# Kernel optimization log

Measured on AMD Instinct MI355X. Metric: run time of the kernel, lower is better.

## Reference

```python
import jax, jax.numpy as jnp
import numpy as np

N_ATOMS = 20000
N_PAIRS = 640000
C = 64        # channel width (pp/pi/ii nodes)
NB = 4        # number of radial basis functions


def setup_inputs() -> dict:
    key = jax.random.key(0)
    ks = jax.random.split(key, 24)
    s = 0.05  # keep tanh pre-activations in linear-ish regime
    inp = {
        "ind_2": jax.random.randint(ks[0], (N_PAIRS, 2), 0, N_ATOMS, dtype=jnp.int64)
                 if jax.config.jax_enable_x64 else
                 jax.random.randint(ks[0], (N_PAIRS, 2), 0, N_ATOMS, dtype=jnp.int32),
        "p1": jax.random.normal(ks[1], (N_ATOMS, C), jnp.float32),
        "p3": jax.random.normal(ks[2], (N_ATOMS, 3, C), jnp.float32),
        "diff": jax.random.normal(ks[3], (N_PAIRS, 3), jnp.float32),
        "basis": jax.random.uniform(ks[4], (N_PAIRS, NB), jnp.float32),
        # pp1: FFLayer([C, C], tanh, bias)
        "Wpp1a": jax.random.normal(ks[5], (C, C), jnp.float32) * s,
        "bpp1a": jnp.zeros((C,), jnp.float32),
        "Wpp1b": jax.random.normal(ks[6], (C, C), jnp.float32) * s,
        "bpp1b": jnp.zeros((C,), jnp.float32),
        # pi1: FFLayer([C, C*NB], tanh, bias), input = concat(p1_i, p1_j) -> 2C
        "Wpi1": jax.random.normal(ks[7], (2 * C, C), jnp.float32) * s,
        "bpi1": jnp.zeros((C,), jnp.float32),
        "Wpi2": jax.random.normal(ks[8], (C, C * NB), jnp.float32) * s,
        "bpi2": jnp.zeros((C * NB,), jnp.float32),
        # ii1: FFLayer([C, 3*C], tanh, no bias)
        "Wii1": jax.random.normal(ks[9], (C, C), jnp.float32) * s,
        "Wii2": jax.random.normal(ks[10], (C, 3 * C), jnp.float32) * s,
        # pp3: FFLayer([C, C], linear, no bias)
        "Wpp3a": jax.random.normal(ks[11], (C, C), jnp.float32) * s,
        "Wpp3b": jax.random.normal(ks[12], (C, C), jnp.float32) * s,
        # PIX (weighted): two biasless Dense(C)
        "Wpxi": jax.random.normal(ks[13], (C, C), jnp.float32) * s,
        "Wpxj": jax.random.normal(ks[14], (C, C), jnp.float32) * s,
        # DotLayer (weighted): two biasless Dense(C)
        "Wdi": jax.random.normal(ks[15], (C, C), jnp.float32) * s,
        "Wdj": jax.random.normal(ks[16], (C, C), jnp.float32) * s,
    }
    return inp


def reference(ind_2, p1, p3, diff, basis,
              Wpp1a, bpp1a, Wpp1b, bpp1b,
              Wpi1, bpi1, Wpi2, bpi2,
              Wii1, Wii2, Wpp3a, Wpp3b,
              Wpxi, Wpxj, Wdi, Wdj):
    n_atoms = p1.shape[0]
    i, j = ind_2[:, 0], ind_2[:, 1]

    # pp1: FFLayer (tanh, bias)
    p1h = jnp.tanh(p1 @ Wpp1a + bpp1a)
    p1h = jnp.tanh(p1h @ Wpp1b + bpp1b)

    # PILayer: gather pair endpoints, concat, FF, contract with basis
    inter = jnp.concatenate([p1h[i], p1h[j]], axis=-1)          # (P, 2C)
    inter = jnp.tanh(inter @ Wpi1 + bpi1)                        # (P, C)
    inter = jnp.tanh(inter @ Wpi2 + bpi2)                        # (P, C*NB)
    nb = basis.shape[-1]
    i1 = jnp.einsum('pcb,pb->pc', inter.reshape(-1, Wpi2.shape[-1] // nb, nb), basis)

    # ii1: FFLayer (tanh, no bias), last width 3*C
    i1 = jnp.tanh(i1 @ Wii1)
    i1 = jnp.tanh(i1 @ Wii2)                                     # (P, 3C)
    i1_1, i1_2, i1_3 = jnp.split(i1, 3, axis=-1)

    # ip1: scatter-sum interactions onto center atoms
    p1_new = jax.ops.segment_sum(i1_2, i, num_segments=n_atoms)  # (N, C)

    # pp3: linear biasless FF on equivariant channel dim
    p3h = (p3 @ Wpp3a) @ Wpp3b                                   # (N, 3, C)

    # PIX (weighted): wi(p3_i) + wj(p3_j)
    i3 = p3h[i] @ Wpxi + p3h[j] @ Wpxj                           # (P, 3, C)

    # scale by i1_3, add displacement channel scaled by i1_1
    i3 = i3 * i1_3[:, None, :] + diff[:, :, None] * i1_1[:, None, :]

    # ip3: scatter-sum equivariant interactions
    p3_new = jax.ops.segment_sum(i3, i, num_segments=n_atoms)    # (N, 3, C)

    # weighted dot product over the Cartesian axis
    dot = jnp.einsum('ixr,ixr->ir', p3_new @ Wdi, p3_new @ Wdj)  # (N, C)
    p1t1 = dot + p1_new
    p3t1 = p3_new * p1t1[:, None, :]
    return p1t1, p3t1
```

## Files before the change

### kernel.cpp

```cpp
#include <hip/hip_runtime.h>


typedef _Float16 half8 __attribute__((ext_vector_type(8)));
typedef __fp16 half2t __attribute__((ext_vector_type(2)));
typedef float floatx4 __attribute__((ext_vector_type(4)));

#define MFMA16(a, b, c) __builtin_amdgcn_mfma_f32_16x16x32_f16((a), (b), (c), 0, 0, 0)

#define WSA_OFF 0
#define W3_OFF 98304
#define P1H_OFF 114688
#define P3H_OFF 2674688
#define CNT_OFF 10354688
#define FILL_OFF 10435584
#define OFF_OFF 10516480
#define BSUM_OFF 10597376
#define IIS_OFF 13157888
#define JJS_OFF 15717888
#define BAS_OFF 18277888
#define DIF_OFF 28517888

#define FB_PI1 0
#define FB_PI2 16
#define FB_II1 48
#define FB_II2 56
#define FB_PXI 80
#define FB_PXJ 88

__device__ __forceinline__ float fast_tanh(float x) {
    float t = __expf(2.0f * x);
    return 1.0f - __fdividef(2.0f, t + 1.0f);
}

__device__ __forceinline__ floatx4 tanh4(floatx4 v) {
    floatx4 r;
    r[0] = fast_tanh(v[0]); r[1] = fast_tanh(v[1]);
    r[2] = fast_tanh(v[2]); r[3] = fast_tanh(v[3]);
    return r;
}

__device__ __forceinline__ void pack_can(const floatx4 h[4], half8& lo, half8& hi) {
    half2t dw[8];
#pragma unroll
    for (int t = 0; t < 4; ++t) {
        dw[2 * t]     = __builtin_amdgcn_cvt_pkrtz(h[t][0], h[t][1]);
        dw[2 * t + 1] = __builtin_amdgcn_cvt_pkrtz(h[t][2], h[t][3]);
    }
    union U { half8 v; half2t d[4]; } u;
    u.d[0] = dw[0]; u.d[1] = dw[1]; u.d[2] = dw[2]; u.d[3] = dw[3]; lo = u.v;
    u.d[0] = dw[4]; u.d[1] = dw[5]; u.d[2] = dw[6]; u.d[3] = dw[7]; hi = u.v;
}

__global__ __launch_bounds__(64) void k_pack(
    const float* __restrict__ Wpi1, const float* __restrict__ Wpi2,
    const float* __restrict__ Wii1, const float* __restrict__ Wii2,
    const float* __restrict__ Wpxi, const float* __restrict__ Wpxj,
    _Float16* __restrict__ wsA) {
    int f = blockIdx.x, l = threadIdx.x;
    int q = l >> 4, c15 = l & 15;
    const float* W; int ldn, mt, kb, mode;
    if (f < 16)      { W = Wpi1; ldn = 64;  mt = f >> 2;        kb = f & 3;        mode = 0; }
    else if (f < 48) { W = Wpi2; ldn = 256; mt = (f - 16) >> 1; kb = (f - 16) & 1; mode = 1; }
    else if (f < 56) { W = Wii1; ldn = 64;  mt = (f - 48) >> 1; kb = (f - 48) & 1; mode = 2; }
    else if (f < 80) { W = Wii2; ldn = 192; mt = (f - 56) >> 1; kb = (f - 56) & 1; mode = 1; }
    else if (f < 88) { W = Wpxi; ldn = 64;  mt = (f - 80) >> 1; kb = (f - 80) & 1; mode = 0; }
    else             { W = Wpxj; ldn = 64;  mt = (f - 88) >> 1; kb = (f - 88) & 1; mode = 0; }
#pragma unroll
    for (int e = 0; e < 8; ++e) {
        int k;
        if (mode == 0) k = 32 * kb + 8 * q + e;
        else if (mode == 1) {
            int d = e >> 1, h = e & 1, j = 4 * kb + d;
            k = 16 * (j >> 1) + 4 * q + 2 * (j & 1) + h;
        } else k = 4 * (8 * kb + e) + q;
        wsA[f * 512 + l * 8 + e] = (_Float16)W[k * ldn + 16 * mt + c15];
    }
}

__global__ __launch_bounds__(256) void k_w3(const float* __restrict__ A,
                                            const float* __restrict__ B,
                                            float* __restrict__ W3) {
    int t = threadIdx.x;
#pragma unroll
    for (int e = 0; e < 16; ++e) {
        int idx = t * 16 + e;
        int k = idx >> 6, c = idx & 63;
        float s = 0.f;
        for (int m = 0; m < 64; ++m) s = fmaf(A[k * 64 + m], B[m * 64 + c], s);
        W3[idx] = s;
    }
}

__device__ __forceinline__ void store8(float* dst, const float v[8]) {
    *(float4*)(dst)     = make_float4(v[0], v[1], v[2], v[3]);
    *(float4*)(dst + 4) = make_float4(v[4], v[5], v[6], v[7]);
}
__device__ __forceinline__ void fma8(const float* row, float wv, float acc[8]) {
    float4 x0 = *(const float4*)(row);
    float4 x1 = *(const float4*)(row + 4);
    acc[0] = fmaf(x0.x, wv, acc[0]); acc[1] = fmaf(x0.y, wv, acc[1]);
    acc[2] = fmaf(x0.z, wv, acc[2]); acc[3] = fmaf(x0.w, wv, acc[3]);
    acc[4] = fmaf(x1.x, wv, acc[4]); acc[5] = fmaf(x1.y, wv, acc[5]);
    acc[6] = fmaf(x1.z, wv, acc[6]); acc[7] = fmaf(x1.w, wv, acc[7]);
}

__global__ __launch_bounds__(256) void k_p1h(const float* __restrict__ p1,
                                             const float* __restrict__ Wa,
                                             const float* __restrict__ ba,
                                             const float* __restrict__ Wb,
                                             const float* __restrict__ bb,
                                             _Float16* __restrict__ p1h) {
    __shared__ float act[4][64][8];
    const int w = threadIdx.x >> 6, lane = threadIdx.x & 63;
    const int a0 = blockIdx.x * 32 + w * 8;
    {
        float t[8];
#pragma unroll
        for (int p = 0; p < 8; ++p) t[p] = p1[(a0 + p) * 64 + lane];
        store8(&act[w][lane][0], t);
    }
    __syncthreads();
    float acc[8];
    {
        float bv = ba[lane];
#pragma unroll
        for (int p = 0; p < 8; ++p) acc[p] = bv;
        for (int k = 0; k < 64; ++k) fma8(&act[w][k][0], Wa[k * 64 + lane], acc);
    }
    __syncthreads();
    {
        float t[8];
#pragma unroll
        for (int p = 0; p < 8; ++p) t[p] = fast_tanh(acc[p]);
        store8(&act[w][lane][0], t);
    }
    __syncthreads();
    {
        float bv = bb[lane];
#pragma unroll
        for (int p = 0; p < 8; ++p) acc[p] = bv;
        for (int k = 0; k < 64; ++k) fma8(&act[w][k][0], Wb[k * 64 + lane], acc);
    }
#pragma unroll
    for (int p = 0; p < 8; ++p) p1h[(a0 + p) * 64 + lane] = (_Float16)fast_tanh(acc[p]);
}

__global__ __launch_bounds__(256) void k_rowmm(const float* __restrict__ X,
                                               const float* __restrict__ W,
                                               _Float16* __restrict__ Y) {
    __shared__ float act[4][64][8];
    const int w = threadIdx.x >> 6, lane = threadIdx.x & 63;
    const int r0 = blockIdx.x * 32 + w * 8;
    {
        float t[8];
#pragma unroll
        for (int p = 0; p < 8; ++p) t[p] = X[(r0 + p) * 64 + lane];
        store8(&act[w][lane][0], t);
    }
    __syncthreads();
    float acc[8];
#pragma unroll
    for (int p = 0; p < 8; ++p) acc[p] = 0.f;
    for (int k = 0; k < 64; ++k) fma8(&act[w][k][0], W[k * 64 + lane], acc);
#pragma unroll
    for (int p = 0; p < 8; ++p) Y[(r0 + p) * 64 + lane] = (_Float16)acc[p];
}

__global__ __launch_bounds__(256) void k_hist(const int* __restrict__ ind,
                                              int* __restrict__ cnt, int n) {
    int t = blockIdx.x * 256 + threadIdx.x;
    if (t < n) atomicAdd(&cnt[ind[2 * t]], 1);
}

__global__ __launch_bounds__(256) void k_scan1(const int* __restrict__ cnt,
                                               int* __restrict__ off,
                                               int* __restrict__ bsum, int n) {
    __shared__ int s[256];
    int b = blockIdx.x, t = threadIdx.x, a = b * 256 + t;
    int v = (a < n) ? cnt[a] : 0;
    s[t] = v;
    __syncthreads();
    for (int o = 1; o < 256; o <<= 1) {
        int x = (t >= o) ? s[t - o] : 0;
        __syncthreads();
        s[t] += x;
        __syncthreads();
    }
    off[a] = s[t] - v;
    if (t == 255) bsum[b] = s[255];
}

__global__ __launch_bounds__(64) void k_scan2(int* __restrict__ bsum, int nb) {
    if (threadIdx.x == 0) {
        int r = 0;
        for (int b = 0; b < nb; ++b) { int t = bsum[b]; bsum[b] = r; r += t; }
    }
}

__global__ __launch_bounds__(256) void k_scan3(int* __restrict__ off,
                                               const int* __restrict__ bsum) {
    int a = blockIdx.x * 256 + threadIdx.x;
    off[a] += bsum[blockIdx.x];
}

__global__ __launch_bounds__(256) void k_scatter(const int* __restrict__ ind,
                                                 const int* __restrict__ off,
                                                 int* __restrict__ fill,
                                                 const float* __restrict__ basis,
                                                 const float* __restrict__ diff,
                                                 int* __restrict__ iiS,
                                                 int* __restrict__ jjS,
                                                 float4* __restrict__ basS,
                                                 float4* __restrict__ difS, int n) {
    int t = blockIdx.x * 256 + threadIdx.x;
    if (t < n) {
        int i = ind[2 * t];
        int slot = off[i] + atomicAdd(&fill[i], 1);
        iiS[slot] = i;
        jjS[slot] = ind[2 * t + 1];
        basS[slot] = *(const float4*)(basis + 4 * t);
        difS[slot] = make_float4(diff[3 * t], diff[3 * t + 1], diff[3 * t + 2], 0.f);
    }
}

__global__ __launch_bounds__(64) void k_pairs_s(
    const int* __restrict__ iiS, const int* __restrict__ jjS,
    const float4* __restrict__ basS, const float4* __restrict__ difS,
    const _Float16* __restrict__ p1h, const _Float16* __restrict__ p3h,
    const _Float16* __restrict__ wsA,
    const float* __restrict__ bpi1, const float* __restrict__ bpi2,
    float* __restrict__ outp1, float* __restrict__ outp3) {
    __shared__ float xpose[2][16][68];
    const int lane = threadIdx.x;
    const int p = lane & 15, q = lane >> 4;
    const int sb0 = blockIdx.x * 32;
    const int slot0 = sb0 + p, slot1 = sb0 + 16 + p;
    const int iA0 = iiS[slot0], jA0 = jjS[slot0];
    const int iA1 = iiS[slot1], jA1 = jjS[slot1];

    const half8* A = (const half8*)wsA;

    half8 b1[2][4];
    b1[0][0] = *(const half8*)(p1h + iA0 * 64 + q * 8);
    b1[0][1] = *(const half8*)(p1h + iA0 * 64 + 32 + q * 8);
    b1[0][2] = *(const half8*)(p1h + jA0 * 64 + q * 8);
    b1[0][3] = *(const half8*)(p1h + jA0 * 64 + 32 + q * 8);
    b1[1][0] = *(const half8*)(p1h + iA1 * 64 + q * 8);
    b1[1][1] = *(const half8*)(p1h + iA1 * 64 + 32 + q * 8);
    b1[1][2] = *(const half8*)(p1h + jA1 * 64 + q * 8);
    b1[1][3] = *(const half8*)(p1h + jA1 * 64 + 32 + q * 8);

    floatx4 h1[2][4];
#pragma unroll
    for (int mt = 0; mt < 4; ++mt) {
        floatx4 acc0 = *(const floatx4*)(bpi1 + 16 * mt + 4 * q);
        floatx4 acc1 = acc0;
#pragma unroll
        for (int kb = 0; kb < 4; ++kb) {
            half8 aw = A[(FB_PI1 + mt * 4 + kb) * 64 + lane];
            acc0 = MFMA16(aw, b1[0][kb], acc0);
            acc1 = MFMA16(aw, b1[1][kb], acc1);
        }
        h1[0][mt] = tanh4(acc0);
        h1[1][mt] = tanh4(acc1);
    }

    half8 b2lo[2], b2hi[2];
    pack_can(h1[0], b2lo[0], b2hi[0]);
    pack_can(h1[1], b2lo[1], b2hi[1]);
    float4 bsv0 = basS[slot0], bsv1 = basS[slot1];
    float i1v[2][16];
#pragma unroll
    for (int mt = 0; mt < 16; ++mt) {
        half8 a0 = A[(FB_PI2 + mt * 2 + 0) * 64 + lane];
        half8 a1 = A[(FB_PI2 + mt * 2 + 1) * 64 + lane];
        floatx4 acc0 = *(const floatx4*)(bpi2 + 16 * mt + 4 * q);
        floatx4 acc1 = acc0;
        acc0 = MFMA16(a0, b2lo[0], acc0);
        acc1 = MFMA16(a0, b2lo[1], acc1);
        acc0 = MFMA16(a1, b2hi[0], acc0);
        acc1 = MFMA16(a1, b2hi[1], acc1);
        i1v[0][mt] = fast_tanh(acc0[0]) * bsv0.x + fast_tanh(acc0[1]) * bsv0.y +
                     fast_tanh(acc0[2]) * bsv0.z + fast_tanh(acc0[3]) * bsv0.w;
        i1v[1][mt] = fast_tanh(acc1[0]) * bsv1.x + fast_tanh(acc1[1]) * bsv1.y +
                     fast_tanh(acc1[2]) * bsv1.z + fast_tanh(acc1[3]) * bsv1.w;
    }

    half8 bi[2][2];
#pragma unroll
    for (int g = 0; g < 2; ++g) {
        half2t dw[8];
#pragma unroll
        for (int j = 0; j < 8; ++j)
            dw[j] = __builtin_amdgcn_cvt_pkrtz(i1v[g][2 * j], i1v[g][2 * j + 1]);
        union U { half8 v; half2t d[4]; } u;
        u.d[0] = dw[0]; u.d[1] = dw[1]; u.d[2] = dw[2]; u.d[3] = dw[3]; bi[g][0] = u.v;
        u.d[0] = dw[4]; u.d[1] = dw[5]; u.d[2] = dw[6]; u.d[3] = dw[7]; bi[g][1] = u.v;
    }
    floatx4 h3[2][4];
#pragma unroll
    for (int mt = 0; mt < 4; ++mt) {
        half8 a0 = A[(FB_II1 + mt * 2 + 0) * 64 + lane];
        half8 a1 = A[(FB_II1 + mt * 2 + 1) * 64 + lane];
        floatx4 acc0 = {0.f, 0.f, 0.f, 0.f};
        floatx4 acc1 = {0.f, 0.f, 0.f, 0.f};
        acc0 = MFMA16(a0, bi[0][0], acc0);
        acc1 = MFMA16(a0, bi[1][0], acc1);
        acc0 = MFMA16(a1, bi[0][1], acc0);
        acc1 = MFMA16(a1, bi[1][1], acc1);
        h3[0][mt] = tanh4(acc0);
        h3[1][mt] = tanh4(acc1);
    }

    half8 b4lo[2], b4hi[2];
    pack_can(h3[0], b4lo[0], b4hi[0]);
    pack_can(h3[1], b4lo[1], b4hi[1]);
    floatx4 i11v[2][4], i13v[2][4];
#pragma unroll
    for (int mt = 0; mt < 12; ++mt) {
        half8 a0 = A[(FB_II2 + mt * 2 + 0) * 64 + lane];
        half8 a1 = A[(FB_II2 + mt * 2 + 1) * 64 + lane];
        floatx4 acc0 = {0.f, 0.f, 0.f, 0.f};
        floatx4 acc1 = {0.f, 0.f, 0.f, 0.f};
        acc0 = MFMA16(a0, b4lo[0], acc0);
        acc1 = MFMA16(a0, b4lo[1], acc1);
        acc0 = MFMA16(a1, b4hi[0], acc0);
        acc1 = MFMA16(a1, b4hi[1], acc1);
        floatx4 t0 = tanh4(acc0);
        floatx4 t1 = tanh4(acc1);
        if (mt < 4) { i11v[0][mt] = t0; i11v[1][mt] = t1; }
        else if (mt < 8) {
            int g4 = ((mt - 4) * 4 + q) * 4;
            *(float4*)&xpose[0][p][g4] = make_float4(t0[0], t0[1], t0[2], t0[3]);
            *(float4*)&xpose[1][p][g4] = make_float4(t1[0], t1[1], t1[2], t1[3]);
        } else { i13v[0][mt - 8] = t0; i13v[1][mt - 8] = t1; }
    }

#pragma unroll
    for (int g = 0; g < 2; ++g) {
        float racc = xpose[g][0][lane];
        int cur = iiS[sb0 + g * 16];
#pragma unroll
        for (int pp = 1; pp < 16; ++pp) {
            int aw = iiS[sb0 + g * 16 + pp];
            if (aw != cur) {
                atomicAdd(&outp1[cur * 64 + lane], racc);
                racc = 0.f; cur = aw;
            }
            racc += xpose[g][pp][lane];
        }
        atomicAdd(&outp1[cur * 64 + lane], racc);
    }

    float4 dv0 = difS[slot0], dv1 = difS[slot1];
    float dvs[2][3] = {{dv0.x, dv0.y, dv0.z}, {dv1.x, dv1.y, dv1.z}};
#pragma unroll
    for (int x = 0; x < 3; ++x) {
        half8 bfi[2][2], bfj[2][2];
#pragma unroll
        for (int kb = 0; kb < 2; ++kb) {
            bfi[0][kb] = *(const half8*)(p3h + (iA0 * 3 + x) * 64 + kb * 32 + q * 8);
            bfj[0][kb] = *(const half8*)(p3h + (jA0 * 3 + x) * 64 + kb * 32 + q * 8);
            bfi[1][kb] = *(const half8*)(p3h + (iA1 * 3 + x) * 64 + kb * 32 + q * 8);
            bfj[1][kb] = *(const half8*)(p3h + (jA1 * 3 + x) * 64 + kb * 32 + q * 8);
        }
#pragma unroll
        for (int mt = 0; mt < 4; ++mt) {
            half8 ai0 = A[(FB_PXI + mt * 2 + 0) * 64 + lane];
            half8 ai1 = A[(FB_PXI + mt * 2 + 1) * 64 + lane];
            half8 aj0 = A[(FB_PXJ + mt * 2 + 0) * 64 + lane];
            half8 aj1 = A[(FB_PXJ + mt * 2 + 1) * 64 + lane];
            floatx4 acc0 = {0.f, 0.f, 0.f, 0.f};
            floatx4 acc1 = {0.f, 0.f, 0.f, 0.f};
            acc0 = MFMA16(ai0, bfi[0][0], acc0);
            acc1 = MFMA16(ai0, bfi[1][0], acc1);
            acc0 = MFMA16(ai1, bfi[0][1], acc0);
            acc1 = MFMA16(ai1, bfi[1][1], acc1);
            acc0 = MFMA16(aj0, bfj[0][0], acc0);
            acc1 = MFMA16(aj0, bfj[1][0], acc1);
            acc0 = MFMA16(aj1, bfj[0][1], acc0);
            acc1 = MFMA16(aj1, bfj[1][1], acc1);
            float4 v0, v1;
            v0.x = fmaf(acc0[0], i13v[0][mt][0], dvs[0][x] * i11v[0][mt][0]);
            v0.y = fmaf(acc0[1], i13v[0][mt][1], dvs[0][x] * i11v[0][mt][1]);
            v0.z = fmaf(acc0[2], i13v[0][mt][2], dvs[0][x] * i11v[0][mt][2]);
            v0.w = fmaf(acc0[3], i13v[0][mt][3], dvs[0][x] * i11v[0][mt][3]);
            v1.x = fmaf(acc1[0], i13v[1][mt][0], dvs[1][x] * i11v[1][mt][0]);
            v1.y = fmaf(acc1[1], i13v[1][mt][1], dvs[1][x] * i11v[1][mt][1]);
            v1.z = fmaf(acc1[2], i13v[1][mt][2], dvs[1][x] * i11v[1][mt][2]);
            v1.w = fmaf(acc1[3], i13v[1][mt][3], dvs[1][x] * i11v[1][mt][3]);
            int g4 = (4 * mt + q) * 4;
            *(float4*)&xpose[0][p][g4] = v0;
            *(float4*)&xpose[1][p][g4] = v1;
        }
#pragma unroll
        for (int g = 0; g < 2; ++g) {
            float racc = xpose[g][0][lane];
            int cur = iiS[sb0 + g * 16];
#pragma unroll
            for (int pp = 1; pp < 16; ++pp) {
                int aw = iiS[sb0 + g * 16 + pp];
                if (aw != cur) {
                    atomicAdd(&outp3[cur * 192 + x * 64 + lane], racc);
                    racc = 0.f; cur = aw;
                }
                racc += xpose[g][pp][lane];
            }
            atomicAdd(&outp3[cur * 192 + x * 64 + lane], racc);
        }
    }
}

__global__ __launch_bounds__(256) void k_pairs(
    const int* __restrict__ ind, const _Float16* __restrict__ p1h,
    const _Float16* __restrict__ p3h, const float* __restrict__ diff,
    const float* __restrict__ basis, const _Float16* __restrict__ wsA,
    const float* __restrict__ bpi1, const float* __restrict__ bpi2,
    float* __restrict__ outp1, float* __restrict__ outp3) {
    __shared__ float xpose[4][16][68];
    const int lane = threadIdx.x & 63;
    const int wv = threadIdx.x >> 6;
    const int p = lane & 15, q = lane >> 4;
    const int pbase0 = (blockIdx.x * 4 + wv) * 16;
    const int pair = pbase0 + p;
    const int ii = ind[2 * pair], jj = ind[2 * pair + 1];
    const half8* A = (const half8*)wsA;
    half8 b1[4];
    b1[0] = *(const half8*)(p1h + ii * 64 + q * 8);
    b1[1] = *(const half8*)(p1h + ii * 64 + 32 + q * 8);
    b1[2] = *(const half8*)(p1h + jj * 64 + q * 8);
    b1[3] = *(const half8*)(p1h + jj * 64 + 32 + q * 8);
    floatx4 h1[4];
#pragma unroll
    for (int mt = 0; mt < 4; ++mt) {
        floatx4 acc = *(const floatx4*)(bpi1 + 16 * mt + 4 * q);
#pragma unroll
        for (int kb = 0; kb < 4; ++kb)
            acc = MFMA16(A[(FB_PI1 + mt * 4 + kb) * 64 + lane], b1[kb], acc);
        h1[mt] = tanh4(acc);
    }
    half8 b2lo, b2hi;
    pack_can(h1, b2lo, b2hi);
    floatx4 bs = *(const floatx4*)(basis + pair * 4);
    float i1v[16];
#pragma unroll
    for (int mt = 0; mt < 16; ++mt) {
        floatx4 acc = *(const floatx4*)(bpi2 + 16 * mt + 4 * q);
        acc = MFMA16(A[(FB_PI2 + mt * 2 + 0) * 64 + lane], b2lo, acc);
        acc = MFMA16(A[(FB_PI2 + mt * 2 + 1) * 64 + lane], b2hi, acc);
        i1v[mt] = fast_tanh(acc[0]) * bs[0] + fast_tanh(acc[1]) * bs[1] +
                  fast_tanh(acc[2]) * bs[2] + fast_tanh(acc[3]) * bs[3];
    }
    half8 bi0, bi1;
    {
        half2t dw[8];
#pragma unroll
        for (int j = 0; j < 8; ++j)
            dw[j] = __builtin_amdgcn_cvt_pkrtz(i1v[2 * j], i1v[2 * j + 1]);
        union U { half8 v; half2t d[4]; } u;
        u.d[0] = dw[0]; u.d[1] = dw[1]; u.d[2] = dw[2]; u.d[3] = dw[3]; bi0 = u.v;
        u.d[0] = dw[4]; u.d[1] = dw[5]; u.d[2] = dw[6]; u.d[3] = dw[7]; bi1 = u.v;
    }
    floatx4 h3[4];
#pragma unroll
    for (int mt = 0; mt < 4; ++mt) {
        floatx4 acc = {0.f, 0.f, 0.f, 0.f};
        acc = MFMA16(A[(FB_II1 + mt * 2 + 0) * 64 + lane], bi0, acc);
        acc = MFMA16(A[(FB_II1 + mt * 2 + 1) * 64 + lane], bi1, acc);
        h3[mt] = tanh4(acc);
    }
    half8 b4lo, b4hi;
    pack_can(h3, b4lo, b4hi);
    floatx4 i11[4], i13[4];
#pragma unroll
    for (int mt = 0; mt < 12; ++mt) {
        floatx4 acc = {0.f, 0.f, 0.f, 0.f};
        acc = MFMA16(A[(FB_II2 + mt * 2 + 0) * 64 + lane], b4lo, acc);
        acc = MFMA16(A[(FB_II2 + mt * 2 + 1) * 64 + lane], b4hi, acc);
        floatx4 t = tanh4(acc);
        if (mt < 4) i11[mt] = t;
        else if (mt < 8) {
            int g = (mt - 4) * 4 + q;
            *(float4*)&xpose[wv][p][g * 4] = make_float4(t[0], t[1], t[2], t[3]);
        } else i13[mt - 8] = t;
    }
    half8 bfi[3][2], bfj[3][2];
#pragma unroll
    for (int x = 0; x < 3; ++x) {
#pragma unroll
        for (int kb = 0; kb < 2; ++kb) {
            bfi[x][kb] = *(const half8*)(p3h + (ii * 3 + x) * 64 + kb * 32 + q * 8);
            bfj[x][kb] = *(const half8*)(p3h + (jj * 3 + x) * 64 + kb * 32 + q * 8);
        }
    }
    __syncthreads();
#pragma unroll
    for (int pp = 0; pp < 16; ++pp) {
        int iw = ind[2 * (pbase0 + pp)];
        atomicAdd(&outp1[iw * 64 + lane], xpose[wv][pp][lane]);
    }
    __syncthreads();
    float dvs[3];
    dvs[0] = diff[pair * 3]; dvs[1] = diff[pair * 3 + 1]; dvs[2] = diff[pair * 3 + 2];
#pragma unroll
    for (int x = 0; x < 3; ++x) {
#pragma unroll
        for (int mt = 0; mt < 4; ++mt) {
            half8 ai0 = A[(FB_PXI + mt * 2 + 0) * 64 + lane];
            half8 ai1 = A[(FB_PXI + mt * 2 + 1) * 64 + lane];
            half8 aj0 = A[(FB_PXJ + mt * 2 + 0) * 64 + lane];
            half8 aj1 = A[(FB_PXJ + mt * 2 + 1) * 64 + lane];
            floatx4 acc = {0.f, 0.f, 0.f, 0.f};
            acc = MFMA16(ai0, bfi[x][0], acc);
            acc = MFMA16(ai1, bfi[x][1], acc);
            acc = MFMA16(aj0, bfj[x][0], acc);
            acc = MFMA16(aj1, bfj[x][1], acc);
            float4 v;
            v.x = fmaf(acc[0], i13[mt][0], dvs[x] * i11[mt][0]);
            v.y = fmaf(acc[1], i13[mt][1], dvs[x] * i11[mt][1]);
            v.z = fmaf(acc[2], i13[mt][2], dvs[x] * i11[mt][2]);
            v.w = fmaf(acc[3], i13[mt][3], dvs[x] * i11[mt][3]);
            *(float4*)&xpose[wv][p][(4 * mt + q) * 4] = v;
        }
        __syncthreads();
#pragma unroll
        for (int pp = 0; pp < 16; ++pp) {
            int iw = ind[2 * (pbase0 + pp)];
            atomicAdd(&outp3[iw * 192 + x * 64 + lane], xpose[wv][pp][lane]);
        }
        __syncthreads();
    }
}

__global__ __launch_bounds__(256) void k_final(const float* __restrict__ Wdi,
                                               const float* __restrict__ Wdj,
                                               float* __restrict__ outp1,
                                               float* __restrict__ outp3) {
    __shared__ float act[4][192][8];
    const int w = threadIdx.x >> 6, lane = threadIdx.x & 63;
    const int a0 = blockIdx.x * 32 + w * 8;
    for (int x = 0; x < 3; ++x) {
        float t[8];
#pragma unroll
        for (int p = 0; p < 8; ++p) t[p] = outp3[((a0 + p) * 3 + x) * 64 + lane];
        store8(&act[w][x * 64 + lane][0], t);
    }
    __syncthreads();
    float u0[8], u1[8], u2[8], v0[8], v1[8], v2[8];
#pragma unroll
    for (int p = 0; p < 8; ++p) {
        u0[p] = u1[p] = u2[p] = 0.f;
        v0[p] = v1[p] = v2[p] = 0.f;
    }
    for (int k = 0; k < 64; ++k) {
        float wi = Wdi[k * 64 + lane];
        float wj = Wdj[k * 64 + lane];
        fma8(&act[w][k][0], wi, u0);
        fma8(&act[w][64 + k][0], wi, u1);
        fma8(&act[w][128 + k][0], wi, u2);
        fma8(&act[w][k][0], wj, v0);
        fma8(&act[w][64 + k][0], wj, v1);
        fma8(&act[w][128 + k][0], wj, v2);
    }
#pragma unroll
    for (int p = 0; p < 8; ++p) {
        float dot = u0[p] * v0[p] + u1[p] * v1[p] + u2[p] * v2[p];
        int o1 = (a0 + p) * 64 + lane;
        float p1t = dot + outp1[o1];
        outp1[o1] = p1t;
#pragma unroll
        for (int x = 0; x < 3; ++x) {
            int o3 = ((a0 + p) * 3 + x) * 64 + lane;
            outp3[o3] = act[w][x * 64 + lane][p] * p1t;
        }
    }
}

extern "C" void kernel_launch(void* const* d_in, const int* in_sizes, int n_in,
                              void* d_out, int out_size, void* d_ws, size_t ws_size,
                              hipStream_t stream) {
    const int*   ind   = (const int*)d_in[0];
    const float* p1    = (const float*)d_in[1];
    const float* p3    = (const float*)d_in[2];
    const float* diff  = (const float*)d_in[3];
    const float* basis = (const float*)d_in[4];
    const float* Wpp1a = (const float*)d_in[5];
    const float* bpp1a = (const float*)d_in[6];
    const float* Wpp1b = (const float*)d_in[7];
    const float* bpp1b = (const float*)d_in[8];
    const float* Wpi1  = (const float*)d_in[9];
    const float* bpi1  = (const float*)d_in[10];
    const float* Wpi2  = (const float*)d_in[11];
    const float* bpi2  = (const float*)d_in[12];
    const float* Wii1  = (const float*)d_in[13];
    const float* Wii2  = (const float*)d_in[14];
    const float* Wpp3a = (const float*)d_in[15];
    const float* Wpp3b = (const float*)d_in[16];
    const float* Wpxi  = (const float*)d_in[17];
    const float* Wpxj  = (const float*)d_in[18];
    const float* Wdi   = (const float*)d_in[19];
    const float* Wdj   = (const float*)d_in[20];

    const int n_atoms = in_sizes[1] / 64;
    const int n_pairs = in_sizes[0] / 2;

    float* outp1 = (float*)d_out;
    float* outp3 = outp1 + (size_t)n_atoms * 64;

    char* ws = (char*)d_ws;
    _Float16* wsA  = (_Float16*)(ws + WSA_OFF);
    float*    W3   = (float*)(ws + W3_OFF);
    _Float16* p1h  = (_Float16*)(ws + P1H_OFF);
    _Float16* p3h  = (_Float16*)(ws + P3H_OFF);
    int*      cnt  = (int*)(ws + CNT_OFF);
    int*      fill = (int*)(ws + FILL_OFF);
    int*      offa = (int*)(ws + OFF_OFF);
    int*      bsum = (int*)(ws + BSUM_OFF);
    int*      iiS  = (int*)(ws + IIS_OFF);
    int*      jjS  = (int*)(ws + JJS_OFF);
    float4*   basS = (float4*)(ws + BAS_OFF);
    float4*   difS = (float4*)(ws + DIF_OFF);

    k_pack<<<96, 64, 0, stream>>>(Wpi1, Wpi2, Wii1, Wii2, Wpxi, Wpxj, wsA);
    k_w3<<<1, 256, 0, stream>>>(Wpp3a, Wpp3b, W3);
    k_p1h<<<n_atoms / 32, 256, 0, stream>>>(p1, Wpp1a, bpp1a, Wpp1b, bpp1b, p1h);
    k_rowmm<<<(n_atoms * 3) / 32, 256, 0, stream>>>(p3, W3, p3h);

    (void)hipMemsetAsync(d_out, 0, (size_t)out_size * sizeof(float), stream);

    if (ws_size >= 38757888) {
        const int nb = (n_atoms + 255) / 256;
        (void)hipMemsetAsync(ws + CNT_OFF, 0, 2 * 80896, stream);
        k_hist<<<(n_pairs + 255) / 256, 256, 0, stream>>>(ind, cnt, n_pairs);
        k_scan1<<<nb, 256, 0, stream>>>(cnt, offa, bsum, n_atoms);
        k_scan2<<<1, 64, 0, stream>>>(bsum, nb);
        k_scan3<<<nb, 256, 0, stream>>>(offa, bsum);
        k_scatter<<<(n_pairs + 255) / 256, 256, 0, stream>>>(ind, offa, fill, basis, diff,
                                                             iiS, jjS, basS, difS, n_pairs);
        k_pairs_s<<<n_pairs / 32, 64, 0, stream>>>(iiS, jjS, basS, difS, p1h, p3h,
                                                   wsA, bpi1, bpi2, outp1, outp3);
    } else {
        k_pairs<<<n_pairs / 64, 256, 0, stream>>>(ind, p1h, p3h, diff, basis, wsA,
                                                  bpi1, bpi2, outp1, outp3);
    }

    k_final<<<n_atoms / 32, 256, 0, stream>>>(Wdi, Wdj, outp1, outp3);
}
```

Measured before the change: 499.9 us.

## Precompute per-atom PIX projections and factor the i-term out of pair sums

Adds a per-atom kernel that computes p3h@Wpxi and p3h@Wpxj once per atom into two new fp16 workspace buffers. The pair kernel then drops its per-pair PIX MFMAs. Since each segment shares the same center atom, it accumulates rj*i1_3 + dx*i1_1 per pair plus a running sum of i1_3, and applies the i-side row once per segment. The aim is to remove the redundant per-pair matmul work. In exchange it adds per-lane gathers of j-rows during the segmented reduction, plus a larger workspace requirement. If the workspace is smaller than the new threshold, the unsorted fallback runs instead.

After: 585.2 us. +17.1%, slower.

```diff
diff --git a/kernel.cpp b/kernel.cpp
--- a/kernel.cpp
+++ b/kernel.cpp
@@ -19,6 +19,8 @@
 #define JJS_OFF 15717888
 #define BAS_OFF 18277888
 #define DIF_OFF 28517888
+#define P3HI_OFF 38757888
+#define P3HJ_OFF 46437888
 
 #define FB_PI1 0
 #define FB_PI2 16
@@ -164,6 +166,35 @@
     for (int k = 0; k < 64; ++k) fma8(&act[w][k][0], W[k * 64 + lane], acc);
 #pragma unroll
     for (int p = 0; p < 8; ++p) Y[(r0 + p) * 64 + lane] = (_Float16)acc[p];
+}
+
+__global__ __launch_bounds__(256) void k_rowmm2(const _Float16* __restrict__ X,
+                                                const float* __restrict__ W1,
+                                                const float* __restrict__ W2,
+                                                _Float16* __restrict__ Y1,
+                                                _Float16* __restrict__ Y2) {
+    __shared__ float act[4][64][8];
+    const int w = threadIdx.x >> 6, lane = threadIdx.x & 63;
+    const int r0 = blockIdx.x * 32 + w * 8;
+    {
+        float t[8];
+#pragma unroll
+        for (int p = 0; p < 8; ++p) t[p] = (float)X[(r0 + p) * 64 + lane];
+        store8(&act[w][lane][0], t);
+    }
+    __syncthreads();
+    float acc1[8], acc2[8];
+#pragma unroll
+    for (int p = 0; p < 8; ++p) { acc1[p] = 0.f; acc2[p] = 0.f; }
+    for (int k = 0; k < 64; ++k) {
+        fma8(&act[w][k][0], W1[k * 64 + lane], acc1);
+        fma8(&act[w][k][0], W2[k * 64 + lane], acc2);
+    }
+#pragma unroll
+    for (int p = 0; p < 8; ++p) {
+        Y1[(r0 + p) * 64 + lane] = (_Float16)acc1[p];
+        Y2[(r0 + p) * 64 + lane] = (_Float16)acc2[p];
+    }
 }
 
 __global__ __launch_bounds__(256) void k_hist(const int* __restrict__ ind,
@@ -225,12 +256,12 @@
 
 __global__ __launch_bounds__(64) void k_pairs_s(
     const int* __restrict__ iiS, const int* __restrict__ jjS,
-    const float4* __restrict__ basS, const float4* __restrict__ difS,
-    const _Float16* __restrict__ p1h, const _Float16* __restrict__ p3h,
-    const _Float16* __restrict__ wsA,
+    const float4* __restrict__ basS, const float* __restrict__ difF,
+    const _Float16* __restrict__ p1h, const _Float16* __restrict__ p3hi,
+    const _Float16* __restrict__ p3hj, const _Float16* __restrict__ wsA,
     const float* __restrict__ bpi1, const float* __restrict__ bpi2,
     float* __restrict__ outp1, float* __restrict__ outp3) {
-    __shared__ float xpose[2][16][68];
+    __shared__ float T0[16][68], T1[16][68], T2[16][68];
     const int lane = threadIdx.x;
     const int p = lane & 15, q = lane >> 4;
     const int sb0 = blockIdx.x * 32;
@@ -315,7 +346,7 @@
     half8 b4lo[2], b4hi[2];
     pack_can(h3[0], b4lo[0], b4hi[0]);
     pack_can(h3[1], b4lo[1], b4hi[1]);
-    floatx4 i11v[2][4], i13v[2][4];
+    floatx4 i11v[2][4], i12v[2][4], i13v[2][4];
 #pragma unroll
     for (int mt = 0; mt < 12; ++mt) {
         half8 a0 = A[(FB_II2 + mt * 2 + 0) * 64 + lane];
@@ -328,85 +359,60 @@
         acc1 = MFMA16(a1, b4hi[1], acc1);
         floatx4 t0 = tanh4(acc0);
         floatx4 t1 = tanh4(acc1);
-        if (mt < 4) { i11v[0][mt] = t0; i11v[1][mt] = t1; }
-        else if (mt < 8) {
-            int g4 = ((mt - 4) * 4 + q) * 4;
-            *(float4*)&xpose[0][p][g4] = make_float4(t0[0], t0[1], t0[2], t0[3]);
-            *(float4*)&xpose[1][p][g4] = make_float4(t1[0], t1[1], t1[2], t1[3]);
-        } else { i13v[0][mt - 8] = t0; i13v[1][mt - 8] = t1; }
+        if (mt < 4)      { i11v[0][mt] = t0;     i11v[1][mt] = t1; }
+        else if (mt < 8) { i12v[0][mt - 4] = t0; i12v[1][mt - 4] = t1; }
+        else             { i13v[0][mt - 8] = t0; i13v[1][mt - 8] = t1; }
     }
 
 #pragma unroll
     for (int g = 0; g < 2; ++g) {
-        float racc = xpose[g][0][lane];
-        int cur = iiS[sb0 + g * 16];
-#pragma unroll
-        for (int pp = 1; pp < 16; ++pp) {
-            int aw = iiS[sb0 + g * 16 + pp];
-            if (aw != cur) {
-                atomicAdd(&outp1[cur * 64 + lane], racc);
-                racc = 0.f; cur = aw;
-            }
-            racc += xpose[g][pp][lane];
-        }
-        atomicAdd(&outp1[cur * 64 + lane], racc);
-    }
-
-    float4 dv0 = difS[slot0], dv1 = difS[slot1];
-    float dvs[2][3] = {{dv0.x, dv0.y, dv0.z}, {dv1.x, dv1.y, dv1.z}};
-#pragma unroll
-    for (int x = 0; x < 3; ++x) {
-        half8 bfi[2][2], bfj[2][2];
-#pragma unroll
-        for (int kb = 0; kb < 2; ++kb) {
-            bfi[0][kb] = *(const half8*)(p3h + (iA0 * 3 + x) * 64 + kb * 32 + q * 8);
-            bfj[0][kb] = *(const half8*)(p3h + (jA0 * 3 + x) * 64 + kb * 32 + q * 8);
-            bfi[1][kb] = *(const half8*)(p3h + (iA1 * 3 + x) * 64 + kb * 32 + q * 8);
-            bfj[1][kb] = *(const half8*)(p3h + (jA1 * 3 + x) * 64 + kb * 32 + q * 8);
-        }
+        const int sb = sb0 + g * 16;
 #pragma unroll
         for (int mt = 0; mt < 4; ++mt) {
-            half8 ai0 = A[(FB_PXI + mt * 2 + 0) * 64 + lane];
-            half8 ai1 = A[(FB_PXI + mt * 2 + 1) * 64 + lane];
-            half8 aj0 = A[(FB_PXJ + mt * 2 + 0) * 64 + lane];
-            half8 aj1 = A[(FB_PXJ + mt * 2 + 1) * 64 + lane];
-            floatx4 acc0 = {0.f, 0.f, 0.f, 0.f};
-            floatx4 acc1 = {0.f, 0.f, 0.f, 0.f};
-            acc0 = MFMA16(ai0, bfi[0][0], acc0);
-            acc1 = MFMA16(ai0, bfi[1][0], acc1);
-            acc0 = MFMA16(ai1, bfi[0][1], acc0);
-            acc1 = MFMA16(ai1, bfi[1][1], acc1);
-            acc0 = MFMA16(aj0, bfj[0][0], acc0);
-            acc1 = MFMA16(aj0, bfj[1][0], acc1);
-            acc0 = MFMA16(aj1, bfj[0][1], acc0);
-            acc1 = MFMA16(aj1, bfj[1][1], acc1);
-            float4 v0, v1;
-            v0.x = fmaf(acc0[0], i13v[0][mt][0], dvs[0][x] * i11v[0][mt][0]);
-            v0.y = fmaf(acc0[1], i13v[0][mt][1], dvs[0][x] * i11v[0][mt][1]);
-            v0.z = fmaf(acc0[2], i13v[0][mt][2], dvs[0][x] * i11v[0][mt][2]);
-            v0.w = fmaf(acc0[3], i13v[0][mt][3], dvs[0][x] * i11v[0][mt][3]);
-            v1.x = fmaf(acc1[0], i13v[1][mt][0], dvs[1][x] * i11v[1][mt][0]);
-            v1.y = fmaf(acc1[1], i13v[1][mt][1], dvs[1][x] * i11v[1][mt][1]);
-            v1.z = fmaf(acc1[2], i13v[1][mt][2], dvs[1][x] * i11v[1][mt][2]);
-            v1.w = fmaf(acc1[3], i13v[1][mt][3], dvs[1][x] * i11v[1][mt][3]);
-            int g4 = (4 * mt + q) * 4;
-            *(float4*)&xpose[0][p][g4] = v0;
-            *(float4*)&xpose[1][p][g4] = v1;
-        }
-#pragma unroll
-        for (int g = 0; g < 2; ++g) {
-            float racc = xpose[g][0][lane];
-            int cur = iiS[sb0 + g * 16];
+            int c4 = (mt * 4 + q) * 4;
+            floatx4 v0 = i12v[g][mt];
+            floatx4 v1 = i11v[g][mt];
+            floatx4 v2 = i13v[g][mt];
+            *(float4*)&T0[p][c4] = make_float4(v0[0], v0[1], v0[2], v0[3]);
+            *(float4*)&T1[p][c4] = make_float4(v1[0], v1[1], v1[2], v1[3]);
+            *(float4*)&T2[p][c4] = make_float4(v2[0], v2[1], v2[2], v2[3]);
+        }
+        {
+            float racc = T0[0][lane];
+            int cur = iiS[sb];
 #pragma unroll
             for (int pp = 1; pp < 16; ++pp) {
-                int aw = iiS[sb0 + g * 16 + pp];
+                int aw = iiS[sb + pp];
                 if (aw != cur) {
-                    atomicAdd(&outp3[cur * 192 + x * 64 + lane], racc);
+                    atomicAdd(&outp1[cur * 64 + lane], racc);
                     racc = 0.f; cur = aw;
                 }
-                racc += xpose[g][pp][lane];
+                racc += T0[pp][lane];
             }
-            atomicAdd(&outp3[cur * 192 + x * 64 + lane], racc);
+            atomicAdd(&outp1[cur * 64 + lane], racc);
+        }
+#pragma unroll
+        for (int x = 0; x < 3; ++x) {
+            float racc = 0.f, s13 = 0.f;
+            int cur = iiS[sb];
+#pragma unroll
+            for (int pp = 0; pp < 16; ++pp) {
+                int aw = iiS[sb + pp];
+                if (aw != cur) {
+                    float rowi = (float)p3hi[(cur * 3 + x) * 64 + lane];
+                    atomicAdd(&outp3[cur * 192 + x * 64 + lane], fmaf(rowi, s13, racc));
+                    racc = 0.f; s13 = 0.f; cur = aw;
+                }
+                int jw = jjS[sb + pp];
+                float dx = difF[(sb + pp) * 4 + x];
+                float rj = (float)p3hj[(jw * 3 + x) * 64 + lane];
+                float t13 = T2[pp][lane];
+                racc = fmaf(rj, t13, racc);
+                racc = fmaf(dx, T1[pp][lane], racc);
+                s13 += t13;
+            }
+            float rowi = (float)p3hi[(cur * 3 + x) * 64 + lane];
+            atomicAdd(&outp3[cur * 192 + x * 64 + lane], fmaf(rowi, s13, racc));
         }
     }
 }
@@ -620,6 +626,8 @@
     int*      jjS  = (int*)(ws + JJS_OFF);
     float4*   basS = (float4*)(ws + BAS_OFF);
     float4*   difS = (float4*)(ws + DIF_OFF);
+    _Float16* p3hi = (_Float16*)(ws + P3HI_OFF);
+    _Float16* p3hj = (_Float16*)(ws + P3HJ_OFF);
 
     k_pack<<<96, 64, 0, stream>>>(Wpi1, Wpi2, Wii1, Wii2, Wpxi, Wpxj, wsA);
     k_w3<<<1, 256, 0, stream>>>(Wpp3a, Wpp3b, W3);
@@ -628,7 +636,8 @@
 
     (void)hipMemsetAsync(d_out, 0, (size_t)out_size * sizeof(float), stream);
 
-    if (ws_size >= 38757888) {
+    if (ws_size >= 54117888) {
+        k_rowmm2<<<(n_atoms * 3) / 32, 256, 0, stream>>>(p3h, Wpxi, Wpxj, p3hi, p3hj);
         const int nb = (n_atoms + 255) / 256;
         (void)hipMemsetAsync(ws + CNT_OFF, 0, 2 * 80896, stream);
         k_hist<<<(n_pairs + 255) / 256, 256, 0, stream>>>(ind, cnt, n_pairs);
@@ -637,8 +646,9 @@
         k_scan3<<<nb, 256, 0, stream>>>(offa, bsum);
         k_scatter<<<(n_pairs + 255) / 256, 256, 0, stream>>>(ind, offa, fill, basis, diff,
                                                              iiS, jjS, basS, difS, n_pairs);
-        k_pairs_s<<<n_pairs / 32, 64, 0, stream>>>(iiS, jjS, basS, difS, p1h, p3h,
-                                                   wsA, bpi1, bpi2, outp1, outp3);
+        k_pairs_s<<<n_pairs / 32, 64, 0, stream>>>(iiS, jjS, basS, (const float*)difS,
+                                                   p1h, p3hi, p3hj, wsA, bpi1, bpi2,
+                                                   outp1, outp3);
     } else {
         k_pairs<<<n_pairs / 64, 256, 0, stream>>>(ind, p1h, p3h, diff, basis, wsA,
                                                   bpi1, bpi2, outp1, outp3);
```
